# Kernel optimization log

Hardware: AMD Instinct MI355X
Metric: run time of the kernel (lower is better)

The kernel has to match this reference:

```python
import jax, jax.numpy as jnp
import numpy as np

B, L, C = 256, 197, 768
H = C // 16          # reduction = 16
N_ADAPTERS = 10
EPS = 1e-12


def l2_normalize(x, axis=-1):
    sq = jnp.sum(x * x, axis=axis, keepdims=True)
    return x * jax.lax.rsqrt(jnp.maximum(sq, EPS))


def setup_inputs() -> dict:
    key = jax.random.key(0)
    k0, k1, k2, k3 = jax.random.split(key, 4)
    x_embed = jax.random.normal(k0, (B, L, C), dtype=jnp.float32)
    # torch nn.Linear weights are [out_features, in_features]
    W1 = jax.random.normal(k1, (N_ADAPTERS, H, C), dtype=jnp.float32) * 0.02
    W2 = jax.random.normal(k2, (N_ADAPTERS, C, H), dtype=jnp.float32) * 0.02
    adapter_key = jax.random.normal(k3, (N_ADAPTERS, C), dtype=jnp.float32)
    return {"x_embed": x_embed, "W1": W1, "W2": W2, "adapter_key": adapter_key}


def reference(x_embed, W1, W2, adapter_key):
    b = x_embed.shape[0]
    # embedding_key == 'mean'
    x_mean = jnp.mean(x_embed, axis=1)                 # [B, C]
    key_norm = l2_normalize(adapter_key, axis=1)       # [10, C]
    x_norm = l2_normalize(x_mean, axis=1)              # [B, C]
    similarity = x_norm @ key_norm.T                   # [B, 10]

    # top-1 per sample, then majority vote -> single adapter id for the whole batch.
    per_sample_idx = jnp.argmax(similarity, axis=1)    # [B]
    counts = jax.ops.segment_sum(jnp.ones((b,), jnp.float32), per_sample_idx,
                                 num_segments=N_ADAPTERS)
    major = jnp.argmax(counts)                         # ties -> smallest id, matching torch
    idx = jnp.full((b, 1), major, dtype=jnp.int32)     # out['adapter_idx']

    # Apply the selected adapter (same id for every sample); len(idx[i]) == 1.
    w1 = W1[major]                                     # [H, C]
    w2 = W2[major]                                     # [C, H]
    h = jax.nn.relu(jnp.einsum('blc,hc->blh', x_embed, w1))
    a = jax.nn.relu(jnp.einsum('blh,ch->blc', h, w2))
    bias = x_embed + a                                 # (x + adapter(x)) / 1

    adapter_norm = key_norm[idx]                       # [B, 1, C]
    reduce_sim = jnp.sum(adapter_norm * x_norm[:, None, :]) / b
    return bias, reduce_sim, idx
```

## Files before the change

### kernel.cpp

```cpp
#include <hip/hip_runtime.h>
#include <hip/hip_bf16.h>

#define B_   256
#define L_   197
#define C_   768
#define H_   48
#define NA_  10
#define ROWS (B_ * L_)
#define TR   16
#define XP   776
#define HP   72
#define NBLK (ROWS / TR)
#define OFF_SIM 38731776
#define OFF_IDX 38731777

typedef __attribute__((ext_vector_type(8))) short short8;
typedef __attribute__((ext_vector_type(4))) short short4_t;
typedef __attribute__((ext_vector_type(4))) float f32x4;

static __device__ inline short f2bf(float f) {
    union { float f; unsigned u; } v; v.f = f;
    unsigned r = v.u + 0x7fffu + ((v.u >> 16) & 1u);
    return (short)(r >> 16);
}
static __device__ inline short bfc(float f) {
    __hip_bfloat16 h = __float2bfloat16(f);
    union { __hip_bfloat16 h; short s; } u; u.h = h;
    return u.s;
}
static __device__ inline float bf2f(short s) {
    union { unsigned u; float f; } v;
    v.u = ((unsigned)(unsigned short)s) << 16;
    return v.f;
}

#define GLW(dst, p, OFF) asm volatile("global_load_dwordx4 %0, %1, off offset:" OFF \
    : "=v"(dst) : "v"(p))

__global__ void kw_convert(const float* __restrict__ W1, const float* __restrict__ W2,
                           short* __restrict__ W1b, short* __restrict__ W2b) {
    int i = blockIdx.x * 256 + threadIdx.x;
    if (i < NA_ * H_ * C_)
        W1b[i] = f2bf(W1[i]);
    if (i < NA_ * C_ * 64) {
        int k  = i & 63;
        int nc = i >> 6;
        W2b[i] = (k < H_) ? f2bf(W2[nc * H_ + k]) : (short)0;
    }
}

__global__ void k1a_partial(const float* __restrict__ x, float* __restrict__ partial) {
    int b = blockIdx.x >> 2, seg = blockIdx.x & 3;
    int l0 = seg * 50, l1 = l0 + 50; if (l1 > L_) l1 = L_;
    int t = threadIdx.x;
    const float* xb = x + (size_t)b * L_ * C_ + t * 4;
    float4 s = {0.f, 0.f, 0.f, 0.f};
    #pragma unroll 5
    for (int l = l0; l < l1; ++l) {
        float4 v = *(const float4*)(xb + (size_t)l * C_);
        s.x += v.x; s.y += v.y; s.z += v.z; s.w += v.w;
    }
    *(float4*)(partial + ((size_t)b * 4 + seg) * C_ + t * 4) = s;
}

__global__ void k1b_sims(const float* __restrict__ partial, const float* __restrict__ akey,
                         float* __restrict__ sims) {
    __shared__ float red[21][256];
    int b = blockIdx.x, t = threadIdx.x;
    const float* p = partial + (size_t)b * 4 * C_;
    float m[3];
    #pragma unroll
    for (int j = 0; j < 3; ++j) {
        int c = t + j * 256;
        m[j] = (p[c] + p[C_ + c] + p[2 * C_ + c] + p[3 * C_ + c]) * (1.f / (float)L_);
    }
    red[0][t] = m[0] * m[0] + m[1] * m[1] + m[2] * m[2];
    #pragma unroll
    for (int k = 0; k < NA_; ++k) {
        float kd = 0.f, kq = 0.f;
        #pragma unroll
        for (int j = 0; j < 3; ++j) {
            float kv = akey[k * C_ + t + j * 256];
            kd += m[j] * kv; kq += kv * kv;
        }
        red[1 + k][t] = kd; red[11 + k][t] = kq;
    }
    __syncthreads();
    for (int s = 128; s > 0; s >>= 1) {
        if (t < s) {
            #pragma unroll
            for (int q = 0; q < 21; ++q) red[q][t] += red[q][t + s];
        }
        __syncthreads();
    }
    if (t < NA_) {
        float msq = red[0][0];
        sims[b * NA_ + t] = red[1 + t][0] * rsqrtf(fmaxf(red[11 + t][0], 1e-12f))
                                          * rsqrtf(fmaxf(msq, 1e-12f));
    }
}

__global__ void k2_select(const float* __restrict__ sims, float* __restrict__ out,
                          int* __restrict__ majorp) {
    __shared__ int counts[NA_];
    __shared__ int majorS;
    __shared__ float rs[256];
    int t = threadIdx.x;
    float s[NA_];
    #pragma unroll
    for (int k = 0; k < NA_; ++k) s[k] = sims[t * NA_ + k];
    int best = 0; float bv = s[0];
    #pragma unroll
    for (int k = 1; k < NA_; ++k) { if (s[k] > bv) { bv = s[k]; best = k; } }
    if (t < NA_) counts[t] = 0;
    __syncthreads();
    atomicAdd(&counts[best], 1);
    __syncthreads();
    if (t == 0) {
        int mj = 0, mc = counts[0];
        #pragma unroll
        for (int k = 1; k < NA_; ++k) { if (counts[k] > mc) { mc = counts[k]; mj = k; } }
        majorS = mj; *majorp = mj;
    }
    __syncthreads();
    int mj = majorS;
    rs[t] = s[mj];
    __syncthreads();
    for (int st = 128; st > 0; st >>= 1) { if (t < st) rs[t] += rs[t + st]; __syncthreads(); }
    if (t == 0) out[OFF_SIM] = rs[0] * (1.f / (float)B_);
    out[OFF_IDX + t] = (float)mj;
}

__launch_bounds__(192, 2)
__global__ void k3_apply(const float* __restrict__ x, const short* __restrict__ W1b,
                         const short* __restrict__ W2b, const int* __restrict__ majorp,
                         float* __restrict__ out) {
    __shared__ short xs[TR * XP];
    __shared__ short hs[TR * HP];
    const int major = *majorp;

    int t = threadIdx.x;
    int w = t >> 6, l = t & 63;
    int rbase = blockIdx.x * TR;
    int lo16 = l & 15;
    int g = l >> 4;
    int klane = g * 8;

    {
        const float* xsrc = x + (size_t)rbase * C_ + t * 4;
        const float* b0 = xsrc;
        const float* b1 = xsrc + 2 * C_;
        const float* b2 = xsrc + 4 * C_;
        const float* b3 = xsrc + 6 * C_;
        const float* b4 = xsrc + 8 * C_;
        const float* b5 = xsrc + 10 * C_;
        const float* b6 = xsrc + 12 * C_;
        const float* b7 = xsrc + 14 * C_;
        f32x4 v0, v1, v2, v3, v4, v5, v6, v7, v8, v9, v10, v11, v12, v13, v14, v15;
        GLW(v0,  b0, "0"); GLW(v1,  b0, "3072");
        GLW(v2,  b1, "0"); GLW(v3,  b1, "3072");
        GLW(v4,  b2, "0"); GLW(v5,  b2, "3072");
        GLW(v6,  b3, "0"); GLW(v7,  b3, "3072");
        GLW(v8,  b4, "0"); GLW(v9,  b4, "3072");
        GLW(v10, b5, "0"); GLW(v11, b5, "3072");
        GLW(v12, b6, "0"); GLW(v13, b6, "3072");
        GLW(v14, b7, "0"); GLW(v15, b7, "3072");

#define STROW(ROW, V) { \
        short4_t sb; \
        sb[0] = bfc((V)[0]); sb[1] = bfc((V)[1]); \
        sb[2] = bfc((V)[2]); sb[3] = bfc((V)[3]); \
        *(short4_t*)&xs[(ROW) * XP + t * 4] = sb; }

        asm volatile("s_waitcnt vmcnt(8)"
            : "+v"(v0), "+v"(v1), "+v"(v2), "+v"(v3),
              "+v"(v4), "+v"(v5), "+v"(v6), "+v"(v7));
        __builtin_amdgcn_sched_barrier(0);
        STROW(0, v0) STROW(1, v1) STROW(2, v2) STROW(3, v3)
        STROW(4, v4) STROW(5, v5) STROW(6, v6) STROW(7, v7)
        asm volatile("s_waitcnt vmcnt(0)"
            : "+v"(v8), "+v"(v9), "+v"(v10), "+v"(v11),
              "+v"(v12), "+v"(v13), "+v"(v14), "+v"(v15));
        __builtin_amdgcn_sched_barrier(0);
        STROW(8, v8)   STROW(9, v9)   STROW(10, v10) STROW(11, v11)
        STROW(12, v12) STROW(13, v13) STROW(14, v14) STROW(15, v15)
#undef STROW
    }
    __syncthreads();

    {
        const short* w1p = W1b + major * (H_ * C_) + (size_t)(w * 16 + lo16) * C_ + klane;
        f32x4 acc = {0, 0, 0, 0};
        short8 q0, q1, q2, q3, q4, q5, q6, q7, q8, q9, q10, q11;
        short8 q12, q13, q14, q15, q16, q17, q18, q19, q20, q21, q22, q23;

#define G1STEP(KK, Q) { \
        short8 xa = *(const short8*)&xs[lo16 * XP + (KK) * 32 + klane]; \
        acc = __builtin_amdgcn_mfma_f32_16x16x32_bf16(xa, Q, acc, 0, 0, 0); }

        GLW(q0,  w1p, "0");    GLW(q1,  w1p, "64");   GLW(q2,  w1p, "128");
        GLW(q3,  w1p, "192");  GLW(q4,  w1p, "256");  GLW(q5,  w1p, "320");
        GLW(q6,  w1p, "384");  GLW(q7,  w1p, "448");  GLW(q8,  w1p, "512");
        GLW(q9,  w1p, "576");  GLW(q10, w1p, "640");  GLW(q11, w1p, "704");
        GLW(q12, w1p, "768");  GLW(q13, w1p, "832");  GLW(q14, w1p, "896");
        GLW(q15, w1p, "960");  GLW(q16, w1p, "1024"); GLW(q17, w1p, "1088");
        GLW(q18, w1p, "1152"); GLW(q19, w1p, "1216"); GLW(q20, w1p, "1280");
        GLW(q21, w1p, "1344"); GLW(q22, w1p, "1408"); GLW(q23, w1p, "1472");
        asm volatile("s_waitcnt vmcnt(12)"
            : "+v"(q0), "+v"(q1), "+v"(q2), "+v"(q3), "+v"(q4), "+v"(q5),
              "+v"(q6), "+v"(q7), "+v"(q8), "+v"(q9), "+v"(q10), "+v"(q11));
        __builtin_amdgcn_sched_barrier(0);
        G1STEP(0, q0)  G1STEP(1, q1)  G1STEP(2, q2)  G1STEP(3, q3)
        G1STEP(4, q4)  G1STEP(5, q5)  G1STEP(6, q6)  G1STEP(7, q7)
        G1STEP(8, q8)  G1STEP(9, q9)  G1STEP(10, q10) G1STEP(11, q11)
        asm volatile("s_waitcnt vmcnt(0)"
            : "+v"(q12), "+v"(q13), "+v"(q14), "+v"(q15), "+v"(q16), "+v"(q17),
              "+v"(q18), "+v"(q19), "+v"(q20), "+v"(q21), "+v"(q22), "+v"(q23));
        __builtin_amdgcn_sched_barrier(0);
        G1STEP(12, q12) G1STEP(13, q13) G1STEP(14, q14) G1STEP(15, q15)
        G1STEP(16, q16) G1STEP(17, q17) G1STEP(18, q18) G1STEP(19, q19)
        G1STEP(20, q20) G1STEP(21, q21) G1STEP(22, q22) G1STEP(23, q23)
#undef G1STEP

        #pragma unroll
        for (int q = 0; q < 4; ++q)
            hs[(g * 4 + q) * HP + w * 16 + lo16] = bfc(fmaxf(acc[q], 0.f));
        if (w == 0) {
            short4_t z = {0, 0, 0, 0};
            *(short4_t*)&hs[lo16 * HP + 48 + g * 4] = z;
        }
    }
    __syncthreads();

    {
        short8 hA = *(const short8*)&hs[lo16 * HP + klane];
        short8 hB = *(const short8*)&hs[lo16 * HP + 32 + klane];
        const short* ba = W2b + (size_t)major * (C_ * 64)
                              + (size_t)(w * 16) * 1024 + lo16 * 64 + klane;
        const short* b1 = ba + 2048;
        const short* b2 = ba + 4096;
        const short* b3 = ba + 6144;
        const short* b4 = ba + 8192;
        const short* b5 = ba + 10240;
        const short* b6 = ba + 12288;
        const short* b7 = ba + 14336;
        short8 p0a, p0b, p1a, p1b, p2a, p2b, p3a, p3b;
        short8 p4a, p4b, p5a, p5b, p6a, p6b, p7a, p7b;
        short8 p8a, p8b, p9a, p9b, p10a, p10b, p11a, p11b;
        short8 p12a, p12b, p13a, p13b, p14a, p14b, p15a, p15b;

        GLW(p0a,  ba, "0");    GLW(p0b,  ba, "64");
        GLW(p1a,  ba, "2048"); GLW(p1b,  ba, "2112");
        GLW(p2a,  b1, "0");    GLW(p2b,  b1, "64");
        GLW(p3a,  b1, "2048"); GLW(p3b,  b1, "2112");
        GLW(p4a,  b2, "0");    GLW(p4b,  b2, "64");
        GLW(p5a,  b2, "2048"); GLW(p5b,  b2, "2112");
        GLW(p6a,  b3, "0");    GLW(p6b,  b3, "64");
        GLW(p7a,  b3, "2048"); GLW(p7b,  b3, "2112");
        GLW(p8a,  b4, "0");    GLW(p8b,  b4, "64");
        GLW(p9a,  b4, "2048"); GLW(p9b,  b4, "2112");
        GLW(p10a, b5, "0");    GLW(p10b, b5, "64");
        GLW(p11a, b5, "2048"); GLW(p11b, b5, "2112");
        GLW(p12a, b6, "0");    GLW(p12b, b6, "64");
        GLW(p13a, b6, "2048"); GLW(p13b, b6, "2112");
        GLW(p14a, b7, "0");    GLW(p14b, b7, "64");
        GLW(p15a, b7, "2048"); GLW(p15b, b7, "2112");

        float* outr = out + (size_t)(rbase + lo16) * C_ + w * 256 + g * 4;

#define G2STEP(JJ, P0, P1) { \
        f32x4 acc = {0, 0, 0, 0}; \
        acc = __builtin_amdgcn_mfma_f32_16x16x32_bf16(P0, hA, acc, 0, 0, 0); \
        acc = __builtin_amdgcn_mfma_f32_16x16x32_bf16(P1, hB, acc, 0, 0, 0); \
        short4_t xbv = *(const short4_t*)&xs[lo16 * XP + (w * 16 + (JJ)) * 16 + g * 4]; \
        f32x4 ov; \
        ov[0] = bf2f(xbv[0]) + fmaxf(acc[0], 0.f); \
        ov[1] = bf2f(xbv[1]) + fmaxf(acc[1], 0.f); \
        ov[2] = bf2f(xbv[2]) + fmaxf(acc[2], 0.f); \
        ov[3] = bf2f(xbv[3]) + fmaxf(acc[3], 0.f); \
        *(f32x4*)(outr + (JJ) * 16) = ov; }

        asm volatile("s_waitcnt vmcnt(16)"
            : "+v"(p0a), "+v"(p0b), "+v"(p1a), "+v"(p1b),
              "+v"(p2a), "+v"(p2b), "+v"(p3a), "+v"(p3b),
              "+v"(p4a), "+v"(p4b), "+v"(p5a), "+v"(p5b),
              "+v"(p6a), "+v"(p6b), "+v"(p7a), "+v"(p7b));
        __builtin_amdgcn_sched_barrier(0);
        G2STEP(0, p0a, p0b)   G2STEP(1, p1a, p1b)
        G2STEP(2, p2a, p2b)   G2STEP(3, p3a, p3b)
        G2STEP(4, p4a, p4b)   G2STEP(5, p5a, p5b)
        G2STEP(6, p6a, p6b)   G2STEP(7, p7a, p7b)
        asm volatile("s_waitcnt vmcnt(0)"
            : "+v"(p8a), "+v"(p8b), "+v"(p9a), "+v"(p9b),
              "+v"(p10a), "+v"(p10b), "+v"(p11a), "+v"(p11b),
              "+v"(p12a), "+v"(p12b), "+v"(p13a), "+v"(p13b),
              "+v"(p14a), "+v"(p14b), "+v"(p15a), "+v"(p15b));
        __builtin_amdgcn_sched_barrier(0);
        G2STEP(8, p8a, p8b)   G2STEP(9, p9a, p9b)
        G2STEP(10, p10a, p10b) G2STEP(11, p11a, p11b)
        G2STEP(12, p12a, p12b) G2STEP(13, p13a, p13b)
        G2STEP(14, p14a, p14b) G2STEP(15, p15a, p15b)
#undef G2STEP
    }
}

extern "C" void kernel_launch(void* const* d_in, const int* in_sizes, int n_in,
                              void* d_out, int out_size, void* d_ws, size_t ws_size,
                              hipStream_t stream) {
    const float* x    = (const float*)d_in[0];
    const float* W1   = (const float*)d_in[1];
    const float* W2   = (const float*)d_in[2];
    const float* akey = (const float*)d_in[3];
    float* out = (float*)d_out;

    char* ws = (char*)d_ws;
    short* W1b     = (short*)ws;
    short* W2b     = (short*)(ws + 737280);
    float* partial = (float*)(ws + 1720320);
    float* sims    = (float*)(ws + 4866048);
    int*   majorp  = (int*)(ws + 4876288);

    hipLaunchKernelGGL(kw_convert, dim3(1920), dim3(256), 0, stream, W1, W2, W1b, W2b);
    hipLaunchKernelGGL(k1a_partial, dim3(B_ * 4), dim3(192), 0, stream, x, partial);
    hipLaunchKernelGGL(k1b_sims, dim3(B_), dim3(256), 0, stream, partial, akey, sims);
    hipLaunchKernelGGL(k2_select, dim3(1), dim3(256), 0, stream, sims, out, majorp);
    hipLaunchKernelGGL(k3_apply, dim3(NBLK), dim3(192), 0, stream, x, W1b, W2b, majorp, out);
}
```

Measured before the change: 126.1 us.

## Fuse bf16 cast of x into mean pass and stream bf16 tile via LDS loads

The mean-reduction kernel now also writes a swizzled bf16 copy of x to workspace. The apply kernel then loads that half-size copy directly into LDS with global_load_lds and reads it through an XOR swizzle, instead of re-reading fp32 x and converting it. The W2 loads are issued before the barrier, and the second wait is relaxed to vmcnt(8). The gain depends on trading one fp32 re-read for a bf16 write plus a bf16 read, and it needs enough workspace; otherwise the old path runs.

```diff
diff --git a/kernel.cpp b/kernel.cpp
--- a/kernel.cpp
+++ b/kernel.cpp
@@ -13,6 +13,8 @@
 #define NBLK (ROWS / TR)
 #define OFF_SIM 38731776
 #define OFF_IDX 38731777
+#define XBF_OFF 4876544ull
+#define WS_NEED (XBF_OFF + (unsigned long long)ROWS * 1536ull)
 
 typedef __attribute__((ext_vector_type(8))) short short8;
 typedef __attribute__((ext_vector_type(4))) short short4_t;
@@ -36,6 +38,9 @@
 
 #define GLW(dst, p, OFF) asm volatile("global_load_dwordx4 %0, %1, off offset:" OFF \
     : "=v"(dst) : "v"(p))
+#define GL2LDSB(g, l) __builtin_amdgcn_global_load_lds( \
+    (const __attribute__((address_space(1))) void*)(g), \
+    (__attribute__((address_space(3))) void*)(l), 16, 0, 0)
 
 __global__ void kw_convert(const float* __restrict__ W1, const float* __restrict__ W2,
                            short* __restrict__ W1b, short* __restrict__ W2b) {
@@ -47,6 +52,27 @@
         int nc = i >> 6;
         W2b[i] = (k < H_) ? f2bf(W2[nc * H_ + k]) : (short)0;
     }
+}
+
+__global__ void pre_sum_cast(const float* __restrict__ x, float* __restrict__ partial,
+                             short* __restrict__ xbf) {
+    int b = blockIdx.x >> 2, seg = blockIdx.x & 3;
+    int l0 = seg * 50, l1 = l0 + 50; if (l1 > L_) l1 = L_;
+    int t = threadIdx.x;
+    const float* xb = x + (size_t)b * L_ * C_ + t * 4;
+    char* xbfb = (char*)xbf;
+    float4 s = {0.f, 0.f, 0.f, 0.f};
+    for (int l = l0; l < l1; ++l) {
+        float4 v = *(const float4*)(xb + (size_t)l * C_);
+        s.x += v.x; s.y += v.y; s.z += v.z; s.w += v.w;
+        size_t R = (size_t)b * L_ + l;
+        short4_t sb;
+        sb[0] = bfc(v.x); sb[1] = bfc(v.y); sb[2] = bfc(v.z); sb[3] = bfc(v.w);
+        unsigned cb = ((unsigned)t * 8) ^ (((unsigned)R & 7u) << 4);
+        *(short4_t*)(xbfb + R * 1536 + cb) = sb;
+    }
+    float* p = partial + ((size_t)b * 4 + seg) * C_ + t * 4;
+    *(float4*)p = s;
 }
 
 __global__ void k1a_partial(const float* __restrict__ x, float* __restrict__ partial) {
@@ -132,10 +158,10 @@
 }
 
 __launch_bounds__(192, 2)
-__global__ void k3_apply(const float* __restrict__ x, const short* __restrict__ W1b,
-                         const short* __restrict__ W2b, const int* __restrict__ majorp,
-                         float* __restrict__ out) {
-    __shared__ short xs[TR * XP];
+__global__ void k3b_apply(const short* __restrict__ xbf, const short* __restrict__ W1b,
+                          const short* __restrict__ W2b, const int* __restrict__ majorp,
+                          float* __restrict__ out) {
+    __shared__ short xs[TR * 768];
     __shared__ short hs[TR * HP];
     const int major = *majorp;
 
@@ -145,46 +171,14 @@
     int lo16 = l & 15;
     int g = l >> 4;
     int klane = g * 8;
-
-    {
-        const float* xsrc = x + (size_t)rbase * C_ + t * 4;
-        const float* b0 = xsrc;
-        const float* b1 = xsrc + 2 * C_;
-        const float* b2 = xsrc + 4 * C_;
-        const float* b3 = xsrc + 6 * C_;
-        const float* b4 = xsrc + 8 * C_;
-        const float* b5 = xsrc + 10 * C_;
-        const float* b6 = xsrc + 12 * C_;
-        const float* b7 = xsrc + 14 * C_;
-        f32x4 v0, v1, v2, v3, v4, v5, v6, v7, v8, v9, v10, v11, v12, v13, v14, v15;
-        GLW(v0,  b0, "0"); GLW(v1,  b0, "3072");
-        GLW(v2,  b1, "0"); GLW(v3,  b1, "3072");
-        GLW(v4,  b2, "0"); GLW(v5,  b2, "3072");
-        GLW(v6,  b3, "0"); GLW(v7,  b3, "3072");
-        GLW(v8,  b4, "0"); GLW(v9,  b4, "3072");
-        GLW(v10, b5, "0"); GLW(v11, b5, "3072");
-        GLW(v12, b6, "0"); GLW(v13, b6, "3072");
-        GLW(v14, b7, "0"); GLW(v15, b7, "3072");
-
-#define STROW(ROW, V) { \
-        short4_t sb; \
-        sb[0] = bfc((V)[0]); sb[1] = bfc((V)[1]); \
-        sb[2] = bfc((V)[2]); sb[3] = bfc((V)[3]); \
-        *(short4_t*)&xs[(ROW) * XP + t * 4] = sb; }
-
-        asm volatile("s_waitcnt vmcnt(8)"
-            : "+v"(v0), "+v"(v1), "+v"(v2), "+v"(v3),
-              "+v"(v4), "+v"(v5), "+v"(v6), "+v"(v7));
-        __builtin_amdgcn_sched_barrier(0);
-        STROW(0, v0) STROW(1, v1) STROW(2, v2) STROW(3, v3)
-        STROW(4, v4) STROW(5, v5) STROW(6, v6) STROW(7, v7)
-        asm volatile("s_waitcnt vmcnt(0)"
-            : "+v"(v8), "+v"(v9), "+v"(v10), "+v"(v11),
-              "+v"(v12), "+v"(v13), "+v"(v14), "+v"(v15));
-        __builtin_amdgcn_sched_barrier(0);
-        STROW(8, v8)   STROW(9, v9)   STROW(10, v10) STROW(11, v11)
-        STROW(12, v12) STROW(13, v13) STROW(14, v14) STROW(15, v15)
-#undef STROW
+    const int swz = (lo16 & 7) << 4;
+
+    {
+        const char* src = (const char*)xbf + (size_t)rbase * 1536 + (size_t)l * 16;
+        char* dst = (char*)xs;
+        #pragma unroll
+        for (int j = 0; j < 8; ++j)
+            GL2LDSB(src + (w * 8 + j) * 1024, dst + (w * 8 + j) * 1024);
     }
     __syncthreads();
 
@@ -195,7 +189,7 @@
         short8 q12, q13, q14, q15, q16, q17, q18, q19, q20, q21, q22, q23;
 
 #define G1STEP(KK, Q) { \
-        short8 xa = *(const short8*)&xs[lo16 * XP + (KK) * 32 + klane]; \
+        short8 xa = *(const short8*)((const char*)xs + lo16 * 1536 + (((KK) * 64 + g * 16) ^ swz)); \
         acc = __builtin_amdgcn_mfma_f32_16x16x32_bf16(xa, Q, acc, 0, 0, 0); }
 
         GLW(q0,  w1p, "0");    GLW(q1,  w1p, "64");   GLW(q2,  w1p, "128");
@@ -230,11 +224,8 @@
             *(short4_t*)&hs[lo16 * HP + 48 + g * 4] = z;
         }
     }
-    __syncthreads();
-
-    {
-        short8 hA = *(const short8*)&hs[lo16 * HP + klane];
-        short8 hB = *(const short8*)&hs[lo16 * HP + 32 + klane];
+
+    {
         const short* ba = W2b + (size_t)major * (C_ * 64)
                               + (size_t)(w * 16) * 1024 + lo16 * 64 + klane;
         const short* b1 = ba + 2048;
@@ -266,8 +257,174 @@
         GLW(p14a, b7, "0");    GLW(p14b, b7, "64");
         GLW(p15a, b7, "2048"); GLW(p15b, b7, "2112");
 
+        __syncthreads();
+
+        short8 hA = *(const short8*)&hs[lo16 * HP + klane];
+        short8 hB = *(const short8*)&hs[lo16 * HP + 32 + klane];
         float* outr = out + (size_t)(rbase + lo16) * C_ + w * 256 + g * 4;
 
+#define G2STEP(JJ, P0, P1) { \
+        f32x4 acc = {0, 0, 0, 0}; \
+        acc = __builtin_amdgcn_mfma_f32_16x16x32_bf16(P0, hA, acc, 0, 0, 0); \
+        acc = __builtin_amdgcn_mfma_f32_16x16x32_bf16(P1, hB, acc, 0, 0, 0); \
+        short4_t xbv = *(const short4_t*)((const char*)xs + lo16 * 1536 + \
+                         ((w * 512 + (JJ) * 32 + g * 8) ^ swz)); \
+        f32x4 ov; \
+        ov[0] = bf2f(xbv[0]) + fmaxf(acc[0], 0.f); \
+        ov[1] = bf2f(xbv[1]) + fmaxf(acc[1], 0.f); \
+        ov[2] = bf2f(xbv[2]) + fmaxf(acc[2], 0.f); \
+        ov[3] = bf2f(xbv[3]) + fmaxf(acc[3], 0.f); \
+        *(f32x4*)(outr + (JJ) * 16) = ov; }
+
+        asm volatile("s_waitcnt vmcnt(16)"
+            : "+v"(p0a), "+v"(p0b), "+v"(p1a), "+v"(p1b),
+              "+v"(p2a), "+v"(p2b), "+v"(p3a), "+v"(p3b),
+              "+v"(p4a), "+v"(p4b), "+v"(p5a), "+v"(p5b),
+              "+v"(p6a), "+v"(p6b), "+v"(p7a), "+v"(p7b));
+        __builtin_amdgcn_sched_barrier(0);
+        G2STEP(0, p0a, p0b)   G2STEP(1, p1a, p1b)
+        G2STEP(2, p2a, p2b)   G2STEP(3, p3a, p3b)
+        G2STEP(4, p4a, p4b)   G2STEP(5, p5a, p5b)
+        G2STEP(6, p6a, p6b)   G2STEP(7, p7a, p7b)
+        asm volatile("s_waitcnt vmcnt(8)"
+            : "+v"(p8a), "+v"(p8b), "+v"(p9a), "+v"(p9b),
+              "+v"(p10a), "+v"(p10b), "+v"(p11a), "+v"(p11b),
+              "+v"(p12a), "+v"(p12b), "+v"(p13a), "+v"(p13b),
+              "+v"(p14a), "+v"(p14b), "+v"(p15a), "+v"(p15b));
+        __builtin_amdgcn_sched_barrier(0);
+        G2STEP(8, p8a, p8b)   G2STEP(9, p9a, p9b)
+        G2STEP(10, p10a, p10b) G2STEP(11, p11a, p11b)
+        G2STEP(12, p12a, p12b) G2STEP(13, p13a, p13b)
+        G2STEP(14, p14a, p14b) G2STEP(15, p15a, p15b)
+#undef G2STEP
+    }
+}
+
+__launch_bounds__(192, 2)
+__global__ void k3_apply(const float* __restrict__ x, const short* __restrict__ W1b,
+                         const short* __restrict__ W2b, const int* __restrict__ majorp,
+                         float* __restrict__ out) {
+    __shared__ short xs[TR * XP];
+    __shared__ short hs[TR * HP];
+    const int major = *majorp;
+    int t = threadIdx.x;
+    int w = t >> 6, l = t & 63;
+    int rbase = blockIdx.x * TR;
+    int lo16 = l & 15;
+    int g = l >> 4;
+    int klane = g * 8;
+    {
+        const float* xsrc = x + (size_t)rbase * C_ + t * 4;
+        const float* c0 = xsrc;
+        const float* c1 = xsrc + 2 * C_;
+        const float* c2 = xsrc + 4 * C_;
+        const float* c3 = xsrc + 6 * C_;
+        const float* c4 = xsrc + 8 * C_;
+        const float* c5 = xsrc + 10 * C_;
+        const float* c6 = xsrc + 12 * C_;
+        const float* c7 = xsrc + 14 * C_;
+        f32x4 v0, v1, v2, v3, v4, v5, v6, v7, v8, v9, v10, v11, v12, v13, v14, v15;
+        GLW(v0,  c0, "0"); GLW(v1,  c0, "3072");
+        GLW(v2,  c1, "0"); GLW(v3,  c1, "3072");
+        GLW(v4,  c2, "0"); GLW(v5,  c2, "3072");
+        GLW(v6,  c3, "0"); GLW(v7,  c3, "3072");
+        GLW(v8,  c4, "0"); GLW(v9,  c4, "3072");
+        GLW(v10, c5, "0"); GLW(v11, c5, "3072");
+        GLW(v12, c6, "0"); GLW(v13, c6, "3072");
+        GLW(v14, c7, "0"); GLW(v15, c7, "3072");
+#define STROW(ROW, V) { \
+        short4_t sb; \
+        sb[0] = bfc((V)[0]); sb[1] = bfc((V)[1]); \
+        sb[2] = bfc((V)[2]); sb[3] = bfc((V)[3]); \
+        *(short4_t*)&xs[(ROW) * XP + t * 4] = sb; }
+        asm volatile("s_waitcnt vmcnt(8)"
+            : "+v"(v0), "+v"(v1), "+v"(v2), "+v"(v3),
+              "+v"(v4), "+v"(v5), "+v"(v6), "+v"(v7));
+        __builtin_amdgcn_sched_barrier(0);
+        STROW(0, v0) STROW(1, v1) STROW(2, v2) STROW(3, v3)
+        STROW(4, v4) STROW(5, v5) STROW(6, v6) STROW(7, v7)
+        asm volatile("s_waitcnt vmcnt(0)"
+            : "+v"(v8), "+v"(v9), "+v"(v10), "+v"(v11),
+              "+v"(v12), "+v"(v13), "+v"(v14), "+v"(v15));
+        __builtin_amdgcn_sched_barrier(0);
+        STROW(8, v8)   STROW(9, v9)   STROW(10, v10) STROW(11, v11)
+        STROW(12, v12) STROW(13, v13) STROW(14, v14) STROW(15, v15)
+#undef STROW
+    }
+    __syncthreads();
+    {
+        const short* w1p = W1b + major * (H_ * C_) + (size_t)(w * 16 + lo16) * C_ + klane;
+        f32x4 acc = {0, 0, 0, 0};
+        short8 q0, q1, q2, q3, q4, q5, q6, q7, q8, q9, q10, q11;
+        short8 q12, q13, q14, q15, q16, q17, q18, q19, q20, q21, q22, q23;
+#define G1STEP(KK, Q) { \
+        short8 xa = *(const short8*)&xs[lo16 * XP + (KK) * 32 + klane]; \
+        acc = __builtin_amdgcn_mfma_f32_16x16x32_bf16(xa, Q, acc, 0, 0, 0); }
+        GLW(q0,  w1p, "0");    GLW(q1,  w1p, "64");   GLW(q2,  w1p, "128");
+        GLW(q3,  w1p, "192");  GLW(q4,  w1p, "256");  GLW(q5,  w1p, "320");
+        GLW(q6,  w1p, "384");  GLW(q7,  w1p, "448");  GLW(q8,  w1p, "512");
+        GLW(q9,  w1p, "576");  GLW(q10, w1p, "640");  GLW(q11, w1p, "704");
+        GLW(q12, w1p, "768");  GLW(q13, w1p, "832");  GLW(q14, w1p, "896");
+        GLW(q15, w1p, "960");  GLW(q16, w1p, "1024"); GLW(q17, w1p, "1088");
+        GLW(q18, w1p, "1152"); GLW(q19, w1p, "1216"); GLW(q20, w1p, "1280");
+        GLW(q21, w1p, "1344"); GLW(q22, w1p, "1408"); GLW(q23, w1p, "1472");
+        asm volatile("s_waitcnt vmcnt(12)"
+            : "+v"(q0), "+v"(q1), "+v"(q2), "+v"(q3), "+v"(q4), "+v"(q5),
+              "+v"(q6), "+v"(q7), "+v"(q8), "+v"(q9), "+v"(q10), "+v"(q11));
+        __builtin_amdgcn_sched_barrier(0);
+        G1STEP(0, q0)  G1STEP(1, q1)  G1STEP(2, q2)  G1STEP(3, q3)
+        G1STEP(4, q4)  G1STEP(5, q5)  G1STEP(6, q6)  G1STEP(7, q7)
+        G1STEP(8, q8)  G1STEP(9, q9)  G1STEP(10, q10) G1STEP(11, q11)
+        asm volatile("s_waitcnt vmcnt(0)"
+            : "+v"(q12), "+v"(q13), "+v"(q14), "+v"(q15), "+v"(q16), "+v"(q17),
+              "+v"(q18), "+v"(q19), "+v"(q20), "+v"(q21), "+v"(q22), "+v"(q23));
+        __builtin_amdgcn_sched_barrier(0);
+        G1STEP(12, q12) G1STEP(13, q13) G1STEP(14, q14) G1STEP(15, q15)
+        G1STEP(16, q16) G1STEP(17, q17) G1STEP(18, q18) G1STEP(19, q19)
+        G1STEP(20, q20) G1STEP(21, q21) G1STEP(22, q22) G1STEP(23, q23)
+#undef G1STEP
+        #pragma unroll
+        for (int q = 0; q < 4; ++q)
+            hs[(g * 4 + q) * HP + w * 16 + lo16] = bfc(fmaxf(acc[q], 0.f));
+        if (w == 0) {
+            short4_t z = {0, 0, 0, 0};
+            *(short4_t*)&hs[lo16 * HP + 48 + g * 4] = z;
+        }
+    }
+    __syncthreads();
+    {
+        short8 hA = *(const short8*)&hs[lo16 * HP + klane];
+        short8 hB = *(const short8*)&hs[lo16 * HP + 32 + klane];
+        const short* ba = W2b + (size_t)major * (C_ * 64)
+                              + (size_t)(w * 16) * 1024 + lo16 * 64 + klane;
+        const short* d1 = ba + 2048;
+        const short* d2 = ba + 4096;
+        const short* d3 = ba + 6144;
+        const short* d4 = ba + 8192;
+        const short* d5 = ba + 10240;
+        const short* d6 = ba + 12288;
+        const short* d7 = ba + 14336;
+        short8 p0a, p0b, p1a, p1b, p2a, p2b, p3a, p3b;
+        short8 p4a, p4b, p5a, p5b, p6a, p6b, p7a, p7b;
+        short8 p8a, p8b, p9a, p9b, p10a, p10b, p11a, p11b;
+        short8 p12a, p12b, p13a, p13b, p14a, p14b, p15a, p15b;
+        GLW(p0a,  ba, "0");    GLW(p0b,  ba, "64");
+        GLW(p1a,  ba, "2048"); GLW(p1b,  ba, "2112");
+        GLW(p2a,  d1, "0");    GLW(p2b,  d1, "64");
+        GLW(p3a,  d1, "2048"); GLW(p3b,  d1, "2112");
+        GLW(p4a,  d2, "0");    GLW(p4b,  d2, "64");
+        GLW(p5a,  d2, "2048"); GLW(p5b,  d2, "2112");
+        GLW(p6a,  d3, "0");    GLW(p6b,  d3, "64");
+        GLW(p7a,  d3, "2048"); GLW(p7b,  d3, "2112");
+        GLW(p8a,  d4, "0");    GLW(p8b,  d4, "64");
+        GLW(p9a,  d4, "2048"); GLW(p9b,  d4, "2112");
+        GLW(p10a, d5, "0");    GLW(p10b, d5, "64");
+        GLW(p11a, d5, "2048"); GLW(p11b, d5, "2112");
+        GLW(p12a, d6, "0");    GLW(p12b, d6, "64");
+        GLW(p13a, d6, "2048"); GLW(p13b, d6, "2112");
+        GLW(p14a, d7, "0");    GLW(p14b, d7, "64");
+        GLW(p15a, d7, "2048"); GLW(p15b, d7, "2112");
+        float* outr = out + (size_t)(rbase + lo16) * C_ + w * 256 + g * 4;
 #define G2STEP(JJ, P0, P1) { \
         f32x4 acc = {0, 0, 0, 0}; \
         acc = __builtin_amdgcn_mfma_f32_16x16x32_bf16(P0, hA, acc, 0, 0, 0); \
@@ -279,7 +436,6 @@
         ov[2] = bf2f(xbv[2]) + fmaxf(acc[2], 0.f); \
         ov[3] = bf2f(xbv[3]) + fmaxf(acc[3], 0.f); \
         *(f32x4*)(outr + (JJ) * 16) = ov; }
-
         asm volatile("s_waitcnt vmcnt(16)"
             : "+v"(p0a), "+v"(p0b), "+v"(p1a), "+v"(p1b),
               "+v"(p2a), "+v"(p2b), "+v"(p3a), "+v"(p3b),
@@ -290,7 +446,7 @@
         G2STEP(2, p2a, p2b)   G2STEP(3, p3a, p3b)
         G2STEP(4, p4a, p4b)   G2STEP(5, p5a, p5b)
         G2STEP(6, p6a, p6b)   G2STEP(7, p7a, p7b)
-        asm volatile("s_waitcnt vmcnt(0)"
+        asm volatile("s_waitcnt vmcnt(8)"
             : "+v"(p8a), "+v"(p8b), "+v"(p9a), "+v"(p9b),
               "+v"(p10a), "+v"(p10b), "+v"(p11a), "+v"(p11b),
               "+v"(p12a), "+v"(p12b), "+v"(p13a), "+v"(p13b),
@@ -319,10 +475,18 @@
     float* partial = (float*)(ws + 1720320);
     float* sims    = (float*)(ws + 4866048);
     int*   majorp  = (int*)(ws + 4876288);
+    short* xbf     = (short*)(ws + XBF_OFF);
 
     hipLaunchKernelGGL(kw_convert, dim3(1920), dim3(256), 0, stream, W1, W2, W1b, W2b);
-    hipLaunchKernelGGL(k1a_partial, dim3(B_ * 4), dim3(192), 0, stream, x, partial);
-    hipLaunchKernelGGL(k1b_sims, dim3(B_), dim3(256), 0, stream, partial, akey, sims);
-    hipLaunchKernelGGL(k2_select, dim3(1), dim3(256), 0, stream, sims, out, majorp);
-    hipLaunchKernelGGL(k3_apply, dim3(NBLK), dim3(192), 0, stream, x, W1b, W2b, majorp, out);
-}
+    if (ws_size >= WS_NEED) {
+        hipLaunchKernelGGL(pre_sum_cast, dim3(B_ * 4), dim3(192), 0, stream, x, partial, xbf);
+        hipLaunchKernelGGL(k1b_sims, dim3(B_), dim3(256), 0, stream, partial, akey, sims);
+        hipLaunchKernelGGL(k2_select, dim3(1), dim3(256), 0, stream, sims, out, majorp);
+        hipLaunchKernelGGL(k3b_apply, dim3(NBLK), dim3(192), 0, stream, xbf, W1b, W2b, majorp, out);
+    } else {
+        hipLaunchKernelGGL(k1a_partial, dim3(B_ * 4), dim3(192), 0, stream, x, partial);
+        hipLaunchKernelGGL(k1b_sims, dim3(B_), dim3(256), 0, stream, partial, akey, sims);
+        hipLaunchKernelGGL(k2_select, dim3(1), dim3(256), 0, stream, sims, out, majorp);
+        hipLaunchKernelGGL(k3_apply, dim3(NBLK), dim3(192), 0, stream, x, W1b, W2b, majorp, out);
+    }
+}
```

After: 148.3 us. +17.5%, slower.
